# Kernel optimization log

Measured on AMD Instinct MI355X. Metric: run time of the kernel, lower is better.

## Reference

```python
import jax, jax.numpy as jnp
import numpy as np

TEMPERATURE = 0.1
NUM_POS = 2


def _cross_entropy(logits, labels):
    # mean over batch of -log_softmax(logits)[i, labels[i]]
    logp = jax.nn.log_softmax(logits, axis=-1)
    return -jnp.take_along_axis(logp, labels[:, None], axis=1).mean()


def setup_inputs() -> dict:
    key = jax.random.key(0)
    k1, k2, k3 = jax.random.split(key, 3)
    B, D, Q = 4096, 256, 65536
    embedding = jax.random.normal(k1, (B, D), dtype=jnp.float32)
    preds = jax.random.normal(k2, (B, D), dtype=jnp.float32)
    queue = jax.random.normal(k3, (Q, D), dtype=jnp.float32)
    queue = queue / jnp.linalg.norm(queue, axis=1, keepdims=True)
    return {"embedding": embedding, "preds": preds, "queue": queue}


def reference(embedding, preds, queue):
    B = embedding.shape[0]
    half = B // NUM_POS
    labels = jnp.arange(half)  # single-trainer: dist_rank = 0

    # nearest-neighbor retrieval from the support queue (no-grad in original)
    sim = embedding @ queue.T                      # [B, Q]
    nearest = queue[jnp.argmax(sim, axis=1)]       # [B, D]

    nn_a, nn_b = nearest[:half], nearest[half:]
    preds_a, preds_b = preds[:half], preds[half:]

    logits_ab = (nn_a @ preds_b.T) / TEMPERATURE   # [half, half]
    logits_ba = (nn_b @ preds_a.T) / TEMPERATURE

    loss = _cross_entropy(logits_ab, labels) / 2 + _cross_entropy(logits_ba, labels) / 2
    return loss
```

## Files before the change

### kernel.cpp

```cpp
#include <hip/hip_runtime.h>
#include <hip/hip_bf16.h>
#include <stdint.h>

#define B_ROWS 4096
#define D_K    256
#define Q_ROWS 65536
#define HALF   2048

typedef __bf16 bf16x8 __attribute__((ext_vector_type(8)));
typedef float  f32x4  __attribute__((ext_vector_type(4)));
typedef int    v8i    __attribute__((ext_vector_type(8)));
typedef int    v4i    __attribute__((ext_vector_type(4)));
typedef unsigned short u16x8 __attribute__((ext_vector_type(8)));
typedef const __attribute__((address_space(1))) void* gptr1;
typedef __attribute__((address_space(3))) void* lptr3;

__device__ __forceinline__ unsigned int f32_ordered(float f) {
    unsigned int u = __float_as_uint(f);
    return (u & 0x80000000u) ? ~u : (u | 0x80000000u);
}

__device__ __forceinline__ unsigned short f2bf_rn(float f) {
    unsigned int u = __float_as_uint(f);
    u += 0x7FFFu + ((u >> 16) & 1u);
    return (unsigned short)(u >> 16);
}

#define EMB4  (B_ROWS * D_K / 4)
#define PRED4 (B_ROWS * D_K / 4)
#define QUE4  (Q_ROWS * D_K / 4)
__global__ __launch_bounds__(256) void prep_kernel(const float* __restrict__ emb,
                                                   const float* __restrict__ preds,
                                                   const float* __restrict__ queue,
                                                   unsigned char* __restrict__ emb8,
                                                   unsigned short* __restrict__ preds_bf,
                                                   unsigned char* __restrict__ queue8,
                                                   unsigned long long* __restrict__ amax,
                                                   float* __restrict__ out) {
    int i = blockIdx.x * 256 + threadIdx.x;
    if (i < EMB4) {
        float4 v = ((const float4*)emb)[i];
        int u = __builtin_amdgcn_cvt_pk_fp8_f32(v.x, v.y, 0, false);
        u     = __builtin_amdgcn_cvt_pk_fp8_f32(v.z, v.w, u, true);
        ((int*)emb8)[i] = u;
    } else if (i < EMB4 + PRED4) {
        int off = i - EMB4;
        float4 v = ((const float4*)preds)[off];
        ushort4 o;
        o.x = f2bf_rn(v.x); o.y = f2bf_rn(v.y); o.z = f2bf_rn(v.z); o.w = f2bf_rn(v.w);
        ((ushort4*)preds_bf)[off] = o;
    } else {
        int off = i - EMB4 - PRED4;
        float4 v = ((const float4*)queue)[off];
        int u = __builtin_amdgcn_cvt_pk_fp8_f32(v.x, v.y, 0, false);
        u     = __builtin_amdgcn_cvt_pk_fp8_f32(v.z, v.w, u, true);
        ((int*)queue8)[off] = u;
    }
    if (i < B_ROWS) amax[i] = 0ull;
    if (i == 0) out[0] = 0.f;
}

#define BM 128
#define BN 128
#define NCHUNK 8
#define MFMA_FP8(av, bv, c) \
    __builtin_amdgcn_mfma_scale_f32_16x16x128_f8f6f4((av), (bv), (c), 0, 0, 0, 0x7F7F7F7F, 0, 0x7F7F7F7F)

__global__ __launch_bounds__(256, 2) void sim_argmax_kernel(const unsigned char* __restrict__ A8,
                                                            const unsigned char* __restrict__ B8,
                                                            unsigned long long* __restrict__ amax) {
    __shared__ unsigned char Asw[BM * D_K];
    __shared__ unsigned char Bs0[BN * 128];
    __shared__ unsigned char Bs1[BN * 128];

    const int tid  = threadIdx.x;
    const int wave = tid >> 6;
    const int lane = tid & 63;
    const int l15  = lane & 15;
    const int quad = lane >> 4;

    const int bid  = blockIdx.x;
    const int xcd  = bid & 7;
    const int j    = bid >> 3;
    const int blk_m = (j & 31) * BM;
    const int ngrp  = (j >> 5) * 8 + xcd;
    const int nbase = ngrp * (BN * NCHUNK);

    const int wave_m = (wave >> 1) * 64;
    const int wave_n = (wave & 1) * 64;

    {
        const unsigned char* gA = A8 + (size_t)(blk_m + (tid >> 4)) * D_K
                                     + (((tid & 15) ^ ((tid >> 4) & 15)) << 4);
#pragma unroll
        for (int jj = 0; jj < 8; jj++)
            __builtin_amdgcn_global_load_lds((gptr1)(gA + jj * 4096),
                                             (lptr3)&Asw[jj * 4096 + wave * 1024], 16, 0, 0);
    }

    const unsigned char* gB = B8 + (size_t)(nbase + (tid >> 3)) * D_K
                                 + (((tid & 7) ^ ((tid >> 3) & 7)) << 4);

#define PREFB(T, BS) do {                                                              \
        const int _off = ((T) >> 1) * (32 * D_K * 4) + ((T) & 1) * 128;                \
        _Pragma("unroll")                                                              \
        for (int _j = 0; _j < 4; _j++)                                                 \
            __builtin_amdgcn_global_load_lds((gptr1)(gB + _j * 8192 + _off),           \
                                             (lptr3)&BS[_j * 4096 + wave * 1024], 16, 0, 0); \
    } while (0)

    int Abase[4], Bbase[4];
#pragma unroll
    for (int mi = 0; mi < 4; mi++) Abase[mi] = (wave_m + mi * 16 + l15) * 256;
#pragma unroll
    for (int ni = 0; ni < 4; ni++) Bbase[ni] = (wave_n + ni * 16 + l15) * 128;
    const int pA = (quad * 2) ^ l15;
    const int pB = (quad * 2) ^ (l15 & 7);

    float bestv[4][4];
    int   bestc[4][4];
#pragma unroll
    for (int mi = 0; mi < 4; mi++)
#pragma unroll
        for (int reg = 0; reg < 4; reg++) { bestv[mi][reg] = -1e30f; bestc[mi][reg] = 0; }

    f32x4 acc[4][4];
#pragma unroll
    for (int i = 0; i < 4; i++)
#pragma unroll
        for (int jj = 0; jj < 4; jj++) acc[i][jj] = (f32x4){0.f, 0.f, 0.f, 0.f};

#define COMPUTE(BS, KT) do {                                                           \
        v8i af[4];                                                                     \
        _Pragma("unroll")                                                              \
        for (int mi = 0; mi < 4; mi++) {                                               \
            const int _lo = Abase[mi] + ((pA ^ ((KT) << 3)) << 4);                     \
            v4i _x = *(const v4i*)&Asw[_lo];                                           \
            v4i _y = *(const v4i*)&Asw[_lo ^ 16];                                      \
            af[mi] = __builtin_shufflevector(_x, _y, 0, 1, 2, 3, 4, 5, 6, 7);          \
        }                                                                              \
        _Pragma("unroll")                                                              \
        for (int ni = 0; ni < 4; ni++) {                                               \
            const int _lo = Bbase[ni] + (pB << 4);                                     \
            v4i _x = *(const v4i*)&BS[_lo];                                            \
            v4i _y = *(const v4i*)&BS[_lo ^ 16];                                       \
            v8i bv = __builtin_shufflevector(_x, _y, 0, 1, 2, 3, 4, 5, 6, 7);          \
            _Pragma("unroll")                                                          \
            for (int mi = 0; mi < 4; mi++)                                             \
                acc[mi][ni] = MFMA_FP8(af[mi], bv, acc[mi][ni]);                       \
        }                                                                              \
    } while (0)

    PREFB(0, Bs0);

#pragma unroll 1
    for (int p = 0; p < NCHUNK; ++p) {
        __syncthreads();
        PREFB(2 * p + 1, Bs1);
        COMPUTE(Bs0, 0);
        __syncthreads();
        if (p < NCHUNK - 1) PREFB(2 * p + 2, Bs0);
        COMPUTE(Bs1, 1);

        const int col0 = nbase + p * BN + wave_n + l15;
#pragma unroll
        for (int mi = 0; mi < 4; mi++) {
#pragma unroll
            for (int reg = 0; reg < 4; reg++) {
#pragma unroll
                for (int ni = 0; ni < 4; ni++) {
                    float v = acc[mi][ni][reg];
                    int   c = col0 + ni * 16;
                    if (v > bestv[mi][reg]) { bestv[mi][reg] = v; bestc[mi][reg] = c; }
                }
                acc[mi][0][reg] = 0.f; acc[mi][1][reg] = 0.f;
                acc[mi][2][reg] = 0.f; acc[mi][3][reg] = 0.f;
            }
        }
    }

#pragma unroll
    for (int mi = 0; mi < 4; mi++) {
#pragma unroll
        for (int reg = 0; reg < 4; reg++) {
            unsigned long long key =
                ((unsigned long long)f32_ordered(bestv[mi][reg]) << 32) |
                (unsigned long long)(0xFFFFFFFFu - (unsigned)bestc[mi][reg]);
#pragma unroll
            for (int m = 1; m < 16; m <<= 1) {
                unsigned long long o = __shfl_xor(key, m, 16);
                if (o > key) key = o;
            }
            if (l15 == mi * 4 + reg) {
                int row = blk_m + wave_m + mi * 16 + quad * 4 + reg;
                atomicMax(&amax[row], key);
            }
        }
    }
}

__global__ __launch_bounds__(512) void logits_ce_kernel(const unsigned long long* __restrict__ amax,
                                                        const float* __restrict__ queue_f32,
                                                        const unsigned short* __restrict__ preds_bf,
                                                        float* __restrict__ out) {
    const int gw   = blockIdx.x;
    const int tid  = threadIdx.x;
    const int wave = tid >> 6;
    const int lane = tid & 63;
    const int l15  = lane & 15;
    const int quad = lane >> 4;
    const int h    = gw >> 7;
    const int rowbase = gw * 16;
    const unsigned short* Bbase = preds_bf + (size_t)((1 - h) * HALF) * D_K;

    __shared__ float sm[8][16], sl[8][16], sd[8][16];

    unsigned idx = 0xFFFFFFFFu - (unsigned)(amax[rowbase + l15] & 0xFFFFFFFFull);
    const float* arow = queue_f32 + (size_t)idx * D_K;
    bf16x8 a[8];
#pragma unroll
    for (int kc = 0; kc < 8; kc++) {
        float4 f0 = *(const float4*)(arow + kc * 32 + quad * 8);
        float4 f1 = *(const float4*)(arow + kc * 32 + quad * 8 + 4);
        u16x8 t;
        t[0] = f2bf_rn(f0.x); t[1] = f2bf_rn(f0.y); t[2] = f2bf_rn(f0.z); t[3] = f2bf_rn(f0.w);
        t[4] = f2bf_rn(f1.x); t[5] = f2bf_rn(f1.y); t[6] = f2bf_rn(f1.z); t[7] = f2bf_rn(f1.w);
        a[kc] = *(const bf16x8*)&t;
    }

    float m_run[4], l_run[4], diag[4];
#pragma unroll
    for (int r = 0; r < 4; r++) { m_run[r] = -1e30f; l_run[r] = 0.f; diag[r] = -1e30f; }

    const int tdiag = gw & 127;
    for (int tt = 0; tt < 16; tt++) {
        const int t = wave * 16 + tt;
        f32x4 acc = (f32x4){0.f, 0.f, 0.f, 0.f};
#pragma unroll
        for (int kc = 0; kc < 8; kc++) {
            bf16x8 b = *(const bf16x8*)&Bbase[(size_t)(t * 16 + l15) * D_K + kc * 32 + quad * 8];
            acc = __builtin_amdgcn_mfma_f32_16x16x32_bf16(a[kc], b, acc, 0, 0, 0);
        }
#pragma unroll
        for (int reg = 0; reg < 4; reg++) {
            float v = acc[reg] * 10.0f;
            if (t == tdiag && l15 == quad * 4 + reg) diag[reg] = v;
            float nm = fmaxf(m_run[reg], v);
            l_run[reg] = l_run[reg] * __expf(m_run[reg] - nm) + __expf(v - nm);
            m_run[reg] = nm;
        }
    }
#pragma unroll
    for (int reg = 0; reg < 4; reg++) {
#pragma unroll
        for (int m = 1; m < 16; m <<= 1) {
            float om = __shfl_xor(m_run[reg], m, 16);
            float ol = __shfl_xor(l_run[reg], m, 16);
            float od = __shfl_xor(diag[reg], m, 16);
            float nm = fmaxf(m_run[reg], om);
            l_run[reg] = l_run[reg] * __expf(m_run[reg] - nm) + ol * __expf(om - nm);
            m_run[reg] = nm;
            diag[reg] = fmaxf(diag[reg], od);
        }
        if (l15 == 0) {
            sm[wave][quad * 4 + reg] = m_run[reg];
            sl[wave][quad * 4 + reg] = l_run[reg];
            sd[wave][quad * 4 + reg] = diag[reg];
        }
    }
    __syncthreads();
    if (tid < 16) {
        float M = -1e30f, L = 0.f, Dg = -1e30f;
#pragma unroll
        for (int w = 0; w < 8; w++) {
            float mw = sm[w][tid], lw = sl[w][tid], dw = sd[w][tid];
            float nM = fmaxf(M, mw);
            L = L * __expf(M - nM) + lw * __expf(mw - nM);
            M = nM;
            Dg = fmaxf(Dg, dw);
        }
        float rl = (M + __logf(L)) - Dg;
#pragma unroll
        for (int m = 1; m < 16; m <<= 1) rl += __shfl_xor(rl, m, 16);
        if (tid == 0) atomicAdd(out, rl * (1.0f / (float)B_ROWS));
    }
}

extern "C" void kernel_launch(void* const* d_in, const int* in_sizes, int n_in,
                              void* d_out, int out_size, void* d_ws, size_t ws_size,
                              hipStream_t stream) {
    const float* emb   = (const float*)d_in[0];
    const float* preds = (const float*)d_in[1];
    const float* queue = (const float*)d_in[2];

    char* w = (char*)d_ws;
    unsigned long long* amax  = (unsigned long long*)w;
    unsigned char*  emb8      = (unsigned char*)(w + (1u << 20));
    unsigned short* preds_bf  = (unsigned short*)(w + (2u << 20));
    unsigned char*  queue8    = (unsigned char*)(w + (4u << 20));

    prep_kernel<<<dim3((EMB4 + PRED4 + QUE4) / 256), 256, 0, stream>>>(
        emb, preds, queue, emb8, preds_bf, queue8, amax, (float*)d_out);
    sim_argmax_kernel<<<dim3((B_ROWS / BM) * (Q_ROWS / (BN * NCHUNK))), 256, 0, stream>>>(
        emb8, queue8, amax);
    logits_ce_kernel<<<dim3(B_ROWS / 16), 512, 0, stream>>>(
        amax, queue, preds_bf, (float*)d_out);
}
```

Baseline: 213.8 us.

## Keep A tile in registers and alias LDS to raise occupancy to three blocks

Loads the block's A fragments (both K halves) from LDS into registers once, then reuses the LDS region for the two B double-buffers. Shared memory drops from 64KB to 32KB per block and launch bounds request 3 blocks per CU, aiming to hide load latency with more resident waves. It also removes the repeated A LDS reads from every compute step. In exchange it holds 64 extra VGPRs of A data per lane, which adds register pressure under the tighter launch bound and could cause spills.

```diff
diff --git a/kernel.cpp b/kernel.cpp
--- a/kernel.cpp
+++ b/kernel.cpp
@@ -66,12 +66,10 @@
 #define MFMA_FP8(av, bv, c) \
     __builtin_amdgcn_mfma_scale_f32_16x16x128_f8f6f4((av), (bv), (c), 0, 0, 0, 0x7F7F7F7F, 0, 0x7F7F7F7F)
 
-__global__ __launch_bounds__(256, 2) void sim_argmax_kernel(const unsigned char* __restrict__ A8,
+__global__ __launch_bounds__(256, 3) void sim_argmax_kernel(const unsigned char* __restrict__ A8,
                                                             const unsigned char* __restrict__ B8,
                                                             unsigned long long* __restrict__ amax) {
-    __shared__ unsigned char Asw[BM * D_K];
-    __shared__ unsigned char Bs0[BN * 128];
-    __shared__ unsigned char Bs1[BN * 128];
+    __shared__ unsigned char sh[32768];
 
     const int tid  = threadIdx.x;
     const int wave = tid >> 6;
@@ -95,26 +93,38 @@
 #pragma unroll
         for (int jj = 0; jj < 8; jj++)
             __builtin_amdgcn_global_load_lds((gptr1)(gA + jj * 4096),
-                                             (lptr3)&Asw[jj * 4096 + wave * 1024], 16, 0, 0);
-    }
+                                             (lptr3)&sh[jj * 4096 + wave * 1024], 16, 0, 0);
+    }
+    __syncthreads();
+
+    const int pA = (quad * 2) ^ l15;
+    v8i areg[2][4];
+#pragma unroll
+    for (int kt = 0; kt < 2; kt++) {
+#pragma unroll
+        for (int mi = 0; mi < 4; mi++) {
+            const int _lo = (wave_m + mi * 16 + l15) * 256 + ((pA ^ (kt << 3)) << 4);
+            v4i _x = *(const v4i*)&sh[_lo];
+            v4i _y = *(const v4i*)&sh[_lo ^ 16];
+            areg[kt][mi] = __builtin_shufflevector(_x, _y, 0, 1, 2, 3, 4, 5, 6, 7);
+        }
+    }
+    __syncthreads();
 
     const unsigned char* gB = B8 + (size_t)(nbase + (tid >> 3)) * D_K
                                  + (((tid & 7) ^ ((tid >> 3) & 7)) << 4);
 
-#define PREFB(T, BS) do {                                                              \
+#define PREFB(T, BSOFF) do {                                                           \
         const int _off = ((T) >> 1) * (32 * D_K * 4) + ((T) & 1) * 128;                \
         _Pragma("unroll")                                                              \
         for (int _j = 0; _j < 4; _j++)                                                 \
             __builtin_amdgcn_global_load_lds((gptr1)(gB + _j * 8192 + _off),           \
-                                             (lptr3)&BS[_j * 4096 + wave * 1024], 16, 0, 0); \
+                                             (lptr3)&sh[(BSOFF) + _j * 4096 + wave * 1024], 16, 0, 0); \
     } while (0)
 
-    int Abase[4], Bbase[4];
-#pragma unroll
-    for (int mi = 0; mi < 4; mi++) Abase[mi] = (wave_m + mi * 16 + l15) * 256;
+    int Bbase[4];
 #pragma unroll
     for (int ni = 0; ni < 4; ni++) Bbase[ni] = (wave_n + ni * 16 + l15) * 128;
-    const int pA = (quad * 2) ^ l15;
     const int pB = (quad * 2) ^ (l15 & 7);
 
     float bestv[4][4];
@@ -130,37 +140,29 @@
 #pragma unroll
         for (int jj = 0; jj < 4; jj++) acc[i][jj] = (f32x4){0.f, 0.f, 0.f, 0.f};
 
-#define COMPUTE(BS, KT) do {                                                           \
-        v8i af[4];                                                                     \
-        _Pragma("unroll")                                                              \
-        for (int mi = 0; mi < 4; mi++) {                                               \
-            const int _lo = Abase[mi] + ((pA ^ ((KT) << 3)) << 4);                     \
-            v4i _x = *(const v4i*)&Asw[_lo];                                           \
-            v4i _y = *(const v4i*)&Asw[_lo ^ 16];                                      \
-            af[mi] = __builtin_shufflevector(_x, _y, 0, 1, 2, 3, 4, 5, 6, 7);          \
-        }                                                                              \
+#define COMPUTE(BSOFF, KT) do {                                                        \
         _Pragma("unroll")                                                              \
         for (int ni = 0; ni < 4; ni++) {                                               \
-            const int _lo = Bbase[ni] + (pB << 4);                                     \
-            v4i _x = *(const v4i*)&BS[_lo];                                            \
-            v4i _y = *(const v4i*)&BS[_lo ^ 16];                                       \
+            const int _lo = (BSOFF) + Bbase[ni] + (pB << 4);                           \
+            v4i _x = *(const v4i*)&sh[_lo];                                            \
+            v4i _y = *(const v4i*)&sh[_lo ^ 16];                                       \
             v8i bv = __builtin_shufflevector(_x, _y, 0, 1, 2, 3, 4, 5, 6, 7);          \
             _Pragma("unroll")                                                          \
             for (int mi = 0; mi < 4; mi++)                                             \
-                acc[mi][ni] = MFMA_FP8(af[mi], bv, acc[mi][ni]);                       \
+                acc[mi][ni] = MFMA_FP8(areg[KT][mi], bv, acc[mi][ni]);                 \
         }                                                                              \
     } while (0)
 
-    PREFB(0, Bs0);
+    PREFB(0, 0);
 
 #pragma unroll 1
     for (int p = 0; p < NCHUNK; ++p) {
         __syncthreads();
-        PREFB(2 * p + 1, Bs1);
-        COMPUTE(Bs0, 0);
+        PREFB(2 * p + 1, 16384);
+        COMPUTE(0, 0);
         __syncthreads();
-        if (p < NCHUNK - 1) PREFB(2 * p + 2, Bs0);
-        COMPUTE(Bs1, 1);
+        if (p < NCHUNK - 1) PREFB(2 * p + 2, 0);
+        COMPUTE(16384, 1);
 
         const int col0 = nbase + p * BN + wave_n + l15;
 #pragma unroll
```

Result: slower. 250.0 us (+16.9%).
